# Performance work log

Hardware: AMD Instinct MI355X
Metric: run time of the kernel (lower is better)

The kernel has to match this reference:

```python
import jax, jax.numpy as jnp
import numpy as np

C1, C2, K, R = 32, 16, 3, 2
N, H, W, D = 2, 32, 32, 32


def _conv3d(x, w, b, pad):
    y = jax.lax.conv_general_dilated(
        x, w, window_strides=(1, 1, 1), padding=[(pad, pad)] * 3,
        dimension_numbers=('NCDHW', 'OIDHW', 'NCDHW'))
    return y + b[None, :, None, None, None]


def setup_inputs() -> dict:
    key = jax.random.key(0)
    ks = jax.random.split(key, 4)
    def winit(k, sh, fan):
        return jax.random.normal(k, sh, jnp.float32) * (1.0 / np.sqrt(fan))
    cm = C1 // 4
    ck = R ** 3 * K ** 3
    return {
        'x': jax.random.normal(ks[0], (N, C1, H, W, D), jnp.float32),
        'w_down': winit(ks[1], (cm, C1, 1, 1, 1), C1),
        'b_down': jnp.zeros((cm,), jnp.float32),
        'w_enc': winit(ks[2], (ck, cm, K, K, K), cm * K ** 3),
        'b_enc': jnp.zeros((ck,), jnp.float32),
        'w_out': winit(ks[3], (C2, C1, 1, 1, 1), C1),
        'b_out': jnp.zeros((C2,), jnp.float32),
    }


def reference(x, w_down, b_down, w_enc, b_enc, w_out, b_out):
    k3, r3 = K ** 3, R ** 3
    n, c, h, wd, d = x.shape
    # kernel prediction branch
    t = _conv3d(x, w_down, b_down, 0)                       # [N, C/4, H, W, D]
    enc = _conv3d(t, w_enc, b_enc, K // 2)                  # [N, r^3*k^3, H, W, D]
    # pixel_shuffle(k^3 outer, r^3 inner) + softmax over k^3 + unfold-back == this:
    kern = enc.reshape(n, k3, r3, h, wd, d)
    kern = jax.nn.softmax(kern, axis=1)
    kern = kern.transpose(0, 3, 4, 5, 1, 2)                 # [N, H, W, D, k^3, r^3]
    # im2col of x, same flattening order as torch triple unfold (kh outer, kd inner)
    p = K // 2
    xp = jnp.pad(x, ((0, 0), (0, 0), (p, p), (p, p), (p, p)))
    patches = jnp.stack(
        [xp[:, :, i:i + h, j:j + wd, l:l + d]
         for i in range(K) for j in range(K) for l in range(K)],
        axis=-1)                                            # [N, C, H, W, D, k^3]
    out = jnp.einsum('nchwdk,nhwdkr->nchwdr', patches, kern)  # [N, C, H, W, D, r^3]
    # pixel shuffle 3D (channel layout: C outer, r^3 inner)
    out = out.reshape(n, c, h, wd, d, R, R, R)
    out = out.transpose(0, 1, 2, 5, 3, 6, 4, 7).reshape(n, c, h * R, wd * R, d * R)
    return _conv3d(out, w_out, b_out, 0)                    # [N, C2, H*R, W*R, D*R]
```

## Files before the change

kernel.cpp:

```cpp
#include <hip/hip_runtime.h>


typedef short bf16x8 __attribute__((ext_vector_type(8)));
typedef float f32x4 __attribute__((ext_vector_type(4)));
typedef float v2f __attribute__((ext_vector_type(2)));

#define PSTR 232
#define PSTRD 116
#define MSP 41616
#define HSP 1224
#define WSP 36

__device__ inline unsigned short f2b(float f) {
  union { float f; unsigned int i; } x;
  x.f = f;
  unsigned int u = x.i;
  return (unsigned short)((u + 0x7FFFu + ((u >> 16) & 1u)) >> 16);
}
__device__ inline v2f b2f2(unsigned int u) {
  union { unsigned int i; float f; } lo, hi;
  lo.i = u << 16;
  hi.i = u & 0xFFFF0000u;
  return (v2f){lo.f, hi.f};
}

__global__ __launch_bounds__(256) void setup_kernel(
    const float* __restrict__ x, const float* __restrict__ w_down,
    const float* __restrict__ b_down, const float* __restrict__ w_enc,
    const float* __restrict__ b_enc, const float* __restrict__ w_out,
    unsigned short* __restrict__ t, uint2* __restrict__ xo64,
    unsigned short* __restrict__ Wb) {
  int blk = blockIdx.x;
  if (blk < 256) {
    int idx = blk * 256 + threadIdx.x;
    int n = idx >> 15, p = idx & 32767;
    int h = p >> 10, w = (p >> 5) & 31, d = p & 31;
    const float* xp = x + ((size_t)n << 20) + p;
    float at[8], ao[16];
#pragma unroll
    for (int m = 0; m < 8; ++m) at[m] = b_down[m];
#pragma unroll
    for (int o = 0; o < 16; ++o) ao[o] = 0.f;
#pragma unroll
    for (int c = 0; c < 32; ++c) {
      float xv = xp[(size_t)c << 15];
#pragma unroll
      for (int m = 0; m < 8; ++m) at[m] = fmaf(xv, w_down[m * 32 + c], at[m]);
#pragma unroll
      for (int o = 0; o < 16; ++o) ao[o] = fmaf(xv, w_out[o * 32 + c], ao[o]);
    }
    size_t spt = (size_t)(h + 1) * HSP + (size_t)(w + 1) * WSP + (d + 2);
#pragma unroll
    for (int m = 0; m < 8; ++m) t[(size_t)(n * 8 + m) * MSP + spt] = f2b(at[m]);
    size_t spx = (size_t)(h + 1) * HSP + (size_t)(w + 1) * WSP + (d + 1);
#pragma unroll
    for (int cq = 0; cq < 4; ++cq) {
      unsigned lo = (unsigned)f2b(ao[4 * cq]) | ((unsigned)f2b(ao[4 * cq + 1]) << 16);
      unsigned hi = (unsigned)f2b(ao[4 * cq + 2]) | ((unsigned)f2b(ao[4 * cq + 3]) << 16);
      xo64[(size_t)(n * 4 + cq) * MSP + spx] = make_uint2(lo, hi);
    }
  } else {
    int i = (blk - 256) * 256 + threadIdx.x;
    if (i < 224 * 224) {
      int o = i / 224;
      int k = i - o * 224;
      float v = 0.f;
      if (o < 216) {
        if (k < 216) v = w_enc[o * 216 + k];
        else if (k == 216) v = b_enc[o];
      }
      Wb[i] = f2b(v);
    }
  }
}

__global__ __launch_bounds__(512, 4) void carafe_kernel(
    const unsigned short* __restrict__ tg, const uint2* __restrict__ xog,
    const unsigned short* __restrict__ Wb, const float* __restrict__ b_out,
    float* __restrict__ y) {
  __shared__ __align__(16) unsigned short p_lds[128 * PSTR];
  __shared__ __align__(16) unsigned int t32[1920];
  __shared__ __align__(16) uint2 xo_lds[1728];

  unsigned int* p32 = (unsigned int*)p_lds;

  int pb = blockIdx.x;
  int n = pb >> 8;
  int h0 = ((pb >> 4) & 15) << 1;
  int w0 = ((pb >> 1) & 7) << 2;
  int d0 = (pb & 1) << 4;
  int tid = threadIdx.x;

  if (tid < 192) {
    int m = tid / 24;
    int rem = tid - m * 24;
    int z = rem / 6;
    int yy = rem - z * 6;
    size_t gsrc = (size_t)(n * 8 + m) * MSP + (size_t)(h0 + z) * HSP +
                  (size_t)(w0 + yy) * WSP + d0;
    uint4 A = *(const uint4*)(tg + gsrc);
    uint4 B = *(const uint4*)(tg + gsrc + 8);
    uint2 C = *(const uint2*)(tg + gsrc + 16);
    unsigned a[10] = {A.x, A.y, A.z, A.w, B.x, B.y, B.z, B.w, C.x, C.y};
    int dst = tid * 10;
#pragma unroll
    for (int j = 0; j < 9; ++j) t32[dst + j] = (a[j] >> 16) | (a[j + 1] << 16);
  } else if (tid < 288) {
    int rr = tid - 192;
    size_t gsrc = (size_t)(n * 4 + (rr / 24)) * MSP +
                  (size_t)(h0 + ((rr / 6) & 3)) * HSP +
                  (size_t)(w0 + (rr % 6)) * WSP + d0;
    int dst = rr * 18;
#pragma unroll
    for (int j = 0; j < 9; ++j)
      *(uint4*)&xo_lds[dst + 2 * j] = *(const uint4*)(xog + gsrc + 2 * j);
  }
  __syncthreads();

  int lane = tid & 63;
  int wv = __builtin_amdgcn_readfirstlane(tid >> 6);

  if (tid < 256) {
    int vp = tid >> 2, kq = tid & 3;
    int vA = vp * 2;
    int vz = vA >> 6, vy = (vA >> 4) & 3, vxh = (vA & 15) >> 1;
    unsigned int outA[27], outB[27];
#pragma unroll
    for (int j = 0; j < 27; ++j) { outA[j] = 0u; outB[j] = 0u; }
#pragma unroll
    for (int mi = 0; mi < 2; ++mi) {
      int m = kq * 2 + mi;
#pragma unroll
      for (int kh = 0; kh < 3; ++kh)
#pragma unroll
        for (int kw = 0; kw < 3; ++kw) {
          int rb = ((m * 4 + vz + kh) * 6 + (vy + kw)) * 10 + vxh;
          unsigned ux = t32[rb], uy = t32[rb + 1];
          unsigned sA[3] = {ux & 0xFFFFu, ux >> 16, uy & 0xFFFFu};
          unsigned sB[3] = {ux >> 16, uy & 0xFFFFu, uy >> 16};
          int kl0 = mi * 27 + kh * 9 + kw * 3;
#pragma unroll
          for (int kd = 0; kd < 3; ++kd) {
            int kl = kl0 + kd;
            outA[kl >> 1] |= sA[kd] << (16 * (kl & 1));
            outB[kl >> 1] |= sB[kd] << (16 * (kl & 1));
          }
        }
    }
    unsigned int* pA = p32 + vA * PSTRD + kq * 27;
    unsigned int* pB = pA + PSTRD;
#pragma unroll
    for (int j = 0; j < 27; ++j) { pA[j] = outA[j]; pB[j] = outB[j]; }
  }
  if (tid < 128) {
    unsigned int* r = p32 + tid * PSTRD;
    r[108] = 0x3F80u;
    r[109] = 0u; r[110] = 0u; r[111] = 0u;
  }
  __syncthreads();

  int l15 = lane & 15;
  int quad = lane >> 4;
  int mh = wv >> 2;
  int nh = wv & 3;

  f32x4 acc[7][2];
#pragma unroll
  for (int i = 0; i < 7; ++i)
#pragma unroll
    for (int j = 0; j < 2; ++j) acc[i][j] = (f32x4){0.f, 0.f, 0.f, 0.f};
  {
    const unsigned short* Arow = Wb + (mh * 112 + l15) * 224 + quad * 8;
    const unsigned short* Bp = p_lds + (nh * 32 + l15) * PSTR + quad * 8;
#pragma unroll
    for (int kt = 0; kt < 7; ++kt) {
      bf16x8 bf0 = *(const bf16x8*)(Bp + kt * 32);
      bf16x8 bf1 = *(const bf16x8*)(Bp + 16 * PSTR + kt * 32);
#pragma unroll
      for (int i = 0; i < 7; ++i) {
        bf16x8 af = *(const bf16x8*)(Arow + i * 16 * 224 + kt * 32);
        acc[i][0] = __builtin_amdgcn_mfma_f32_16x16x32_bf16(af, bf0, acc[i][0], 0, 0, 0);
        acc[i][1] = __builtin_amdgcn_mfma_f32_16x16x32_bf16(af, bf1, acc[i][1], 0, 0, 0);
      }
    }
  }
  __syncthreads();

#pragma unroll
  for (int i = 0; i < 7; ++i) {
    int o = (mh * 7 + i) * 16 + quad * 4;
    if (o < 216) {
#pragma unroll
      for (int jn = 0; jn < 2; ++jn) {
        int vv = nh * 32 + jn * 16 + l15;
        unsigned lo = (unsigned)f2b(acc[i][jn][0]) | ((unsigned)f2b(acc[i][jn][1]) << 16);
        unsigned hi = (unsigned)f2b(acc[i][jn][2]) | ((unsigned)f2b(acc[i][jn][3]) << 16);
        *(uint2*)&p_lds[vv * PSTR + o] = make_uint2(lo, hi);
      }
    }
  }
  __syncthreads();

  {
    int vv = tid >> 2, rp = tid & 3;
    unsigned int* e = p32 + vv * PSTRD + rp;
    float v0[27], v1[27];
    float mx0 = -3.0e38f, mx1 = -3.0e38f;
#pragma unroll
    for (int k = 0; k < 27; ++k) {
      v2f f = b2f2(e[k * 4]);
      v0[k] = f.x; v1[k] = f.y;
      mx0 = fmaxf(mx0, f.x);
      mx1 = fmaxf(mx1, f.y);
    }
    float s0 = 0.f, s1 = 0.f;
#pragma unroll
    for (int k = 0; k < 27; ++k) {
      v0[k] = __expf(v0[k] - mx0);
      v1[k] = __expf(v1[k] - mx1);
      s0 += v0[k];
      s1 += v1[k];
    }
    float i0 = 1.0f / s0, i1 = 1.0f / s1;
#pragma unroll
    for (int k = 0; k < 27; ++k)
      e[k * 4] = (unsigned)f2b(v0[k] * i0) | ((unsigned)f2b(v1[k] * i1) << 16);
  }
  __syncthreads();

  int cq = wv >> 1;
  int v4 = ((wv & 1) << 6) | lane;
  int vz = v4 >> 6, vy = (v4 >> 4) & 3, vx = v4 & 15;
  v2f accy[4][4];
#pragma unroll
  for (int i = 0; i < 4; ++i) {
    float bo = b_out[cq * 4 + i];
#pragma unroll
    for (int j = 0; j < 4; ++j) accy[i][j] = (v2f){bo, bo};
  }
  const unsigned short* kb = p_lds + v4 * PSTR;
#pragma unroll
  for (int kh = 0; kh < 3; ++kh)
#pragma unroll
    for (int kw = 0; kw < 3; ++kw)
#pragma unroll
      for (int kd = 0; kd < 3; ++kd) {
        int k = kh * 9 + kw * 3 + kd;
        int off = ((cq * 4 + vz + kh) * 6 + (vy + kw)) * 18 + (vx + kd);
        uint4 kw4 = *(const uint4*)(kb + k * 8);
        v2f kr[4];
        kr[0] = b2f2(kw4.x);
        kr[1] = b2f2(kw4.y);
        kr[2] = b2f2(kw4.z);
        kr[3] = b2f2(kw4.w);
        uint2 xq = xo_lds[off];
        v2f x01 = b2f2(xq.x), x23 = b2f2(xq.y);
        float xv[4] = {x01.x, x01.y, x23.x, x23.y};
#pragma unroll
        for (int i = 0; i < 4; ++i) {
          v2f xs = (v2f){xv[i], xv[i]};
#pragma unroll
          for (int j = 0; j < 4; ++j)
            accy[i][j] = __builtin_elementwise_fma(xs, kr[j], accy[i][j]);
        }
      }

  int hh = (h0 + vz) << 1, ww = (w0 + vy) << 1, dd = (d0 + vx) << 1;
#pragma unroll
  for (int i = 0; i < 4; ++i) {
    size_t cb = ((size_t)(n * 16 + cq * 4 + i)) << 18;
#pragma unroll
    for (int rh = 0; rh < 2; ++rh)
#pragma unroll
      for (int rw = 0; rw < 2; ++rw) {
        v2f a = accy[i][rh * 2 + rw];
        *(float2*)&y[cb + (size_t)((hh + rh) << 12) + ((ww + rw) << 6) + dd] =
            make_float2(a.x, a.y);
      }
  }
}

extern "C" void kernel_launch(void* const* d_in, const int* in_sizes, int n_in,
                              void* d_out, int out_size, void* d_ws, size_t ws_size,
                              hipStream_t stream) {
  const float* x      = (const float*)d_in[0];
  const float* w_down = (const float*)d_in[1];
  const float* b_down = (const float*)d_in[2];
  const float* w_enc  = (const float*)d_in[3];
  const float* b_enc  = (const float*)d_in[4];
  const float* w_out  = (const float*)d_in[5];
  const float* b_out  = (const float*)d_in[6];
  float* y = (float*)d_out;

  char* ws = (char*)d_ws;
  unsigned short* t    = (unsigned short*)(ws);
  uint2*          xo64 = (uint2*)(ws + 2663424);
  unsigned short* Wb   = (unsigned short*)(ws + 5326848);

  setup_kernel<<<dim3(452), dim3(256), 0, stream>>>(x, w_down, b_down, w_enc,
                                                    b_enc, w_out, t, xo64, Wb);
  carafe_kernel<<<dim3(512), dim3(512), 0, stream>>>(t, xo64, Wb, b_out, y);
}
```

Before: 113.1 us.

## Fuse softmax into MFMA accumulators by giving each wave all output channels

The MFMA tiling changes so each wave owns 16 voxels and all 224 output rows, instead of a 2x4 split over rows and voxels. The softmax then runs directly on the accumulator registers, using a cross-lane shuffle to combine the two halves. This removes one LDS write/read round trip and one barrier, and the softmax input stays in fp32 instead of being rounded to bf16 first. In exchange each wave reloads the full weight matrix and holds 14 accumulators, which raises register pressure and the number of A-operand loads per wave.

```diff
diff --git a/kernel.cpp b/kernel.cpp
--- a/kernel.cpp
+++ b/kernel.cpp
@@ -161,70 +161,55 @@
 
   int l15 = lane & 15;
   int quad = lane >> 4;
-  int mh = wv >> 2;
-  int nh = wv & 3;
-
-  f32x4 acc[7][2];
-#pragma unroll
-  for (int i = 0; i < 7; ++i)
-#pragma unroll
-    for (int j = 0; j < 2; ++j) acc[i][j] = (f32x4){0.f, 0.f, 0.f, 0.f};
+
+  f32x4 acc[14];
+#pragma unroll
+  for (int i = 0; i < 14; ++i) acc[i] = (f32x4){0.f, 0.f, 0.f, 0.f};
   {
-    const unsigned short* Arow = Wb + (mh * 112 + l15) * 224 + quad * 8;
-    const unsigned short* Bp = p_lds + (nh * 32 + l15) * PSTR + quad * 8;
+    const unsigned short* Bp = p_lds + (wv * 16 + l15) * PSTR + quad * 8;
+    const unsigned short* Aw = Wb + l15 * 224 + quad * 8;
 #pragma unroll
     for (int kt = 0; kt < 7; ++kt) {
-      bf16x8 bf0 = *(const bf16x8*)(Bp + kt * 32);
-      bf16x8 bf1 = *(const bf16x8*)(Bp + 16 * PSTR + kt * 32);
-#pragma unroll
-      for (int i = 0; i < 7; ++i) {
-        bf16x8 af = *(const bf16x8*)(Arow + i * 16 * 224 + kt * 32);
-        acc[i][0] = __builtin_amdgcn_mfma_f32_16x16x32_bf16(af, bf0, acc[i][0], 0, 0, 0);
-        acc[i][1] = __builtin_amdgcn_mfma_f32_16x16x32_bf16(af, bf1, acc[i][1], 0, 0, 0);
-      }
-    }
-  }
-  __syncthreads();
-
-#pragma unroll
-  for (int i = 0; i < 7; ++i) {
-    int o = (mh * 7 + i) * 16 + quad * 4;
-    if (o < 216) {
-#pragma unroll
-      for (int jn = 0; jn < 2; ++jn) {
-        int vv = nh * 32 + jn * 16 + l15;
-        unsigned lo = (unsigned)f2b(acc[i][jn][0]) | ((unsigned)f2b(acc[i][jn][1]) << 16);
-        unsigned hi = (unsigned)f2b(acc[i][jn][2]) | ((unsigned)f2b(acc[i][jn][3]) << 16);
-        *(uint2*)&p_lds[vv * PSTR + o] = make_uint2(lo, hi);
-      }
-    }
-  }
-  __syncthreads();
+      bf16x8 bf = *(const bf16x8*)(Bp + kt * 32);
+#pragma unroll
+      for (int i = 0; i < 14; ++i) {
+        bf16x8 af = *(const bf16x8*)(Aw + i * 16 * 224 + kt * 32);
+        acc[i] = __builtin_amdgcn_mfma_f32_16x16x32_bf16(af, bf, acc[i], 0, 0, 0);
+      }
+    }
+  }
 
   {
-    int vv = tid >> 2, rp = tid & 3;
-    unsigned int* e = p32 + vv * PSTRD + rp;
-    float v0[27], v1[27];
-    float mx0 = -3.0e38f, mx1 = -3.0e38f;
-#pragma unroll
-    for (int k = 0; k < 27; ++k) {
-      v2f f = b2f2(e[k * 4]);
-      v0[k] = f.x; v1[k] = f.y;
-      mx0 = fmaxf(mx0, f.x);
-      mx1 = fmaxf(mx1, f.y);
-    }
-    float s0 = 0.f, s1 = 0.f;
-#pragma unroll
-    for (int k = 0; k < 27; ++k) {
-      v0[k] = __expf(v0[k] - mx0);
-      v1[k] = __expf(v1[k] - mx1);
-      s0 += v0[k];
-      s1 += v1[k];
-    }
-    float i0 = 1.0f / s0, i1 = 1.0f / s1;
-#pragma unroll
-    for (int k = 0; k < 27; ++k)
-      e[k * 4] = (unsigned)f2b(v0[k] * i0) | ((unsigned)f2b(v1[k] * i1) << 16);
+    bool odd = quad >= 2;
+    int imax = odd ? 13 : 14;
+#pragma unroll
+    for (int rr = 0; rr < 4; ++rr) {
+      float mx = -3.0e38f;
+      for (int i = 0; i < imax; ++i) mx = fmaxf(mx, acc[i][rr]);
+      mx = fmaxf(mx, __shfl_xor(mx, 32));
+      float s = 0.f;
+      for (int i = 0; i < imax; ++i) {
+        float e = __expf(acc[i][rr] - mx);
+        acc[i][rr] = e;
+        s += e;
+      }
+      s += __shfl_xor(s, 32);
+      float inv = 1.0f / s;
+      for (int i = 0; i < imax; ++i) acc[i][rr] *= inv;
+    }
+  }
+  __syncthreads();
+
+  {
+    int v = wv * 16 + l15;
+#pragma unroll
+    for (int i = 0; i < 14; ++i) {
+      if (i < 13 || quad < 2) {
+        unsigned lo = (unsigned)f2b(acc[i][0]) | ((unsigned)f2b(acc[i][1]) << 16);
+        unsigned hi = (unsigned)f2b(acc[i][2]) | ((unsigned)f2b(acc[i][3]) << 16);
+        *(uint2*)&p_lds[v * PSTR + i * 16 + quad * 4] = make_uint2(lo, hi);
+      }
+    }
   }
   __syncthreads();
 
```

Measured after the change: 235.2 us. 108% more time.
